# Kernel tuning notes

Measured on AMD Instinct MI355X. Metric: run time of the kernel, lower is better.

The kernel has to match this reference:

```python
import jax, jax.numpy as jnp
import numpy as np

H = 128          # hid_feats
IN0, IN1 = 128, 64
OUT = 64         # out_feats
L = 3            # num_layers
N = 50000        # nodes per graph


def _rbf(x, W, b):
    # sklearn RBFSampler: z = sqrt(2/D) * cos(x @ W + b)
    return jnp.sqrt(2.0 / H) * jnp.cos(x @ W + b)


def _sage_branch(feat, src, dst, Wself, Wneigh, bias, n_nodes):
    # deg of each dst node (constant across layers)
    deg = jax.ops.segment_sum(jnp.ones_like(dst, dtype=feat.dtype), dst, n_nodes)
    denom = jnp.maximum(deg, 1.0)[:, None]
    for i in range(Wself.shape[0]):
        s = jax.ops.segment_sum(feat[src], dst, n_nodes)   # gather + scatter-add
        neigh = jnp.where(deg[:, None] > 0, s / denom, 0.0)
        feat = feat @ Wself[i] + neigh @ Wneigh[i] + bias[i]
    return feat


def setup_inputs() -> dict:
    key = jax.random.key(0)
    ks = jax.random.split(key, 20)
    gamma = 0.1
    inp = {}
    inp['feat0'] = jax.random.normal(ks[0], (N, IN0), jnp.float32)
    inp['feat1'] = jax.random.normal(ks[1], (N, IN1), jnp.float32)
    E = 800000
    inp['src0'] = jax.random.randint(ks[2], (E,), 0, N, jnp.int32)
    inp['dst0'] = jax.random.randint(ks[3], (E,), 0, N, jnp.int32)
    inp['src1'] = jax.random.randint(ks[4], (E,), 0, N, jnp.int32)
    inp['dst1'] = jax.random.randint(ks[5], (E,), 0, N, jnp.int32)
    # RBF random Fourier feature params (W ~ sqrt(2*gamma)*N(0,1), b ~ U[0,2pi))
    inp['rbf_W0'] = jnp.sqrt(2 * gamma) * jax.random.normal(ks[6], (IN0, H), jnp.float32)
    inp['rbf_b0'] = jax.random.uniform(ks[7], (H,), jnp.float32, 0.0, 2 * np.pi)
    inp['rbf_W1'] = jnp.sqrt(2 * gamma) * jax.random.normal(ks[8], (IN1, H), jnp.float32)
    inp['rbf_b1'] = jax.random.uniform(ks[9], (H,), jnp.float32, 0.0, 2 * np.pi)
    sc = 1.0 / np.sqrt(H)
    # branch 1 (g1) and branch 2 (g0) SAGEConv params, stacked over layers
    inp['Wself1'] = sc * jax.random.normal(ks[10], (L, H, H), jnp.float32)
    inp['Wneigh1'] = sc * jax.random.normal(ks[11], (L, H, H), jnp.float32)
    inp['b1'] = jnp.zeros((L, H), jnp.float32)
    inp['Wself2'] = sc * jax.random.normal(ks[12], (L, H, H), jnp.float32)
    inp['Wneigh2'] = sc * jax.random.normal(ks[13], (L, H, H), jnp.float32)
    inp['b2'] = jnp.zeros((L, H), jnp.float32)
    inp['fc1_W'] = sc * jax.random.normal(ks[14], (2 * H, H), jnp.float32)
    inp['fc1_b'] = jnp.zeros((H,), jnp.float32)
    inp['out_W'] = sc * jax.random.normal(ks[15], (H, OUT), jnp.float32)
    inp['out_b'] = jnp.zeros((OUT,), jnp.float32)
    inp['ro_W'] = (1.0 / np.sqrt(OUT)) * jax.random.normal(ks[16], (OUT, 1), jnp.float32)
    inp['ro_b'] = jnp.zeros((1,), jnp.float32)
    return inp


def reference(feat0, feat1, src0, dst0, src1, dst1,
              rbf_W0, rbf_b0, rbf_W1, rbf_b1,
              Wself1, Wneigh1, b1, Wself2, Wneigh2, b2,
              fc1_W, fc1_b, out_W, out_b, ro_W, ro_b):
    # branch 1: g1 path-complex features
    h1 = _rbf(feat1, rbf_W1, rbf_b1)
    y1 = _sage_branch(h1, src1, dst1, Wself1, Wneigh1, b1, feat1.shape[0])
    # branch 2: g0 node features
    h0 = _rbf(feat0, rbf_W0, rbf_b0)
    y2 = _sage_branch(h0, src0, dst0, Wself2, Wneigh2, b2, feat0.shape[0])
    # adaptive_avg_pool1d to 1 == mean over nodes
    y = jnp.concatenate([y2.mean(axis=0), y1.mean(axis=0)], axis=0)  # [2H]
    h = jax.nn.relu(y @ fc1_W + fc1_b)          # dropout is identity in eval
    h = jax.nn.leaky_relu(h @ out_W + out_b, negative_slope=0.01)
    return h @ ro_W + ro_b                      # [1]
```

## Files before the change

kernel.cpp:

```cpp
#include <hip/hip_runtime.h>
#include <math.h>

#define HF   128
#define CAPW 64
#define HB   64

__global__ __launch_bounds__(256) void hist_kernel(const int* __restrict__ s0, const int* __restrict__ d0,
                                                   const int* __restrict__ s1, const int* __restrict__ d1,
                                                   unsigned int* __restrict__ cntbuf,
                                                   int N, int E){
  __shared__ unsigned int sm32[12544];
  const int t = threadIdx.x;
  const int HW = (N + 3) >> 2;
  const int b  = blockIdx.x & 63;
  const int br = (blockIdx.x >> 6) & 1;
  const int z  = blockIdx.x >> 7;
  const int* keys = z ? (br ? d1 : d0) : (br ? s1 : s0);
  for (int w = t; w < HW; w += 256) sm32[w] = 0u;
  __syncthreads();
  const int C  = (E + HB - 1) / HB;
  const int lo = b * C;
  int hi = lo + C; if (hi > E) hi = E;
  for (int i = lo + t; i < hi; i += 256){
    int k = keys[i];
    atomicAdd(&sm32[k >> 2], 1u << ((k & 3) << 3));
  }
  __syncthreads();
  unsigned int* out = cntbuf + ((size_t)(z * 2 + br) * HB + b) * HW;
  for (int w = t; w < HW; w += 256) out[w] = sm32[w];
}

__global__ __launch_bounds__(256) void scan_kernel(unsigned int* __restrict__ cntbuf,
                                                   int* __restrict__ deg,
                                                   int* __restrict__ fill,
                                                   double* __restrict__ SG, int N){
  if (blockIdx.x == 0){
    for (int z = threadIdx.x; z < 1056; z += 256) SG[z] = 0.0;
  }
  int k = blockIdx.x * 256 + threadIdx.x;
  if (k >= 2 * N) return;
  const int br = k >= N;
  const int kk = k - br * N;
  const int HW = (N + 3) >> 2;
  unsigned char* cb = (unsigned char*)cntbuf;
  size_t dbase = ((size_t)(2 + br) * HB) * HW * 4 + kk;
  int ds = 0;
  for (int b = 0; b < HB; ++b) ds += cb[dbase + (size_t)b * HW * 4];
  deg[k] = ds;
  size_t sbase = ((size_t)(0 + br) * HB) * HW * 4 + kk;
  int run = 0;
  for (int b = 0; b < HB; ++b){
    size_t a = sbase + (size_t)b * HW * 4;
    int c = cb[a];
    cb[a] = (unsigned char)run;
    run += c;
  }
  fill[k] = run;
}

__global__ __launch_bounds__(256) void scatter_kernel(const int* __restrict__ s0, const int* __restrict__ d0,
                                                      const int* __restrict__ s1, const int* __restrict__ d1,
                                                      const unsigned int* __restrict__ cntbuf,
                                                      unsigned short* __restrict__ slots,
                                                      int N, int E){
  __shared__ unsigned int sm32[6272];
  const int t  = threadIdx.x;
  const int b  = blockIdx.x & 63;
  const int br = (blockIdx.x >> 6) & 1;
  const int h  = blockIdx.x >> 7;
  const int HW = (N + 3) >> 2;
  const int HN = ((N + 7) >> 3) << 2;
  const int klo = h ? HN : 0;
  const int khi = h ? N : HN;
  const int nw  = (khi - klo + 3) >> 2;
  const unsigned int* offw = cntbuf + ((size_t)br * HB + b) * HW + (klo >> 2);
  for (int w = t; w < nw; w += 256) sm32[w] = offw[w];
  __syncthreads();
  const int* srcA = br ? s1 : s0;
  const int* dstA = br ? d1 : d0;
  const int C  = (E + HB - 1) / HB;
  const int lo = b * C;
  int hi = lo + C; if (hi > E) hi = E;
  const size_t obase = (size_t)br * N;
  for (int i = lo + t; i < hi; i += 256){
    int s = srcA[i];
    if (s < klo || s >= khi) continue;
    int d = dstA[i];
    int sl = s - klo;
    unsigned int old = atomicAdd(&sm32[sl >> 2], 1u << ((sl & 3) << 3));
    int j = (old >> ((sl & 3) << 3)) & 0xff;
    if (j < CAPW) slots[(obase + s) * CAPW + j] = (unsigned short)d;
  }
}

__global__ __launch_bounds__(256) void pull1_kernel(const unsigned short* __restrict__ slots,
                                                    const int* __restrict__ fill,
                                                    const int* __restrict__ deg,
                                                    float* __restrict__ w1,
                                                    float* __restrict__ qa,
                                                    double* __restrict__ S, int N){
  int i = blockIdx.x * 256 + threadIdx.x;
  int t = threadIdx.x;
  float a = 0.f;
  int dgi = 0;
  int br = 0;
  bool valid = i < 2 * N;
  if (valid){
    br = i >= N;
    int o = br * N;
    int c = fill[i]; if (c > CAPW) c = CAPW;
    const unsigned short* sl = slots + (size_t)i * CAPW;
    int j = 0;
    for (; j + 7 < c; j += 8){
      int dA = sl[j], dB = sl[j+1], dC = sl[j+2], dD = sl[j+3];
      int dE = sl[j+4], dF = sl[j+5], dG = sl[j+6], dH = sl[j+7];
      a += 1.f/(float)deg[o+dA] + 1.f/(float)deg[o+dB]
         + 1.f/(float)deg[o+dC] + 1.f/(float)deg[o+dD]
         + 1.f/(float)deg[o+dE] + 1.f/(float)deg[o+dF]
         + 1.f/(float)deg[o+dG] + 1.f/(float)deg[o+dH];
    }
    for (; j < c; ++j) a += 1.f/(float)deg[o + sl[j]];
    dgi = deg[i];
    w1[i] = a;
    qa[i] = dgi > 0 ? a * (1.f/(float)dgi) : 0.f;
  }
  __shared__ double rd[4][256];
  bool pos = valid && dgi > 0;
  rd[0][t] = (pos && !br) ? 1.0 : 0.0;
  rd[1][t] = (pos && !br) ? (double)a : 0.0;
  rd[2][t] = (pos &&  br) ? 1.0 : 0.0;
  rd[3][t] = (pos &&  br) ? (double)a : 0.0;
  __syncthreads();
  for (int off = 128; off; off >>= 1){
    if (t < off){
      rd[0][t] += rd[0][t+off]; rd[1][t] += rd[1][t+off];
      rd[2][t] += rd[2][t+off]; rd[3][t] += rd[3][t+off];
    }
    __syncthreads();
  }
  if (t < 4) atomicAdd(&S[t], rd[t][0]);
}

template<bool WQ>
__global__ __launch_bounds__(256) void pull_kernel(const unsigned short* __restrict__ slots,
                                                   const int* __restrict__ fill,
                                                   const int* __restrict__ deg,
                                                   const float* __restrict__ qin,
                                                   float* __restrict__ wout,
                                                   float* __restrict__ qout, int N){
  int i = blockIdx.x * 256 + threadIdx.x;
  if (i >= 2 * N) return;
  int br = i >= N;
  int o = br * N;
  int c = fill[i]; if (c > CAPW) c = CAPW;
  const unsigned short* sl = slots + (size_t)i * CAPW;
  float a = 0.f;
  int j = 0;
  for (; j + 7 < c; j += 8){
    int dA = sl[j], dB = sl[j+1], dC = sl[j+2], dD = sl[j+3];
    int dE = sl[j+4], dF = sl[j+5], dG = sl[j+6], dH = sl[j+7];
    a += qin[o+dA] + qin[o+dB] + qin[o+dC] + qin[o+dD]
       + qin[o+dE] + qin[o+dF] + qin[o+dG] + qin[o+dH];
  }
  for (; j < c; ++j) a += qin[o + sl[j]];
  wout[i] = a;
  if (WQ){
    int dgi = deg[i];
    qout[i] = dgi > 0 ? a * (1.f/(float)dgi) : 0.f;
  }
}

template<int K1>
__device__ __forceinline__ void gemmred_body(const float* __restrict__ A,
                                             const float* __restrict__ W,
                                             const float* __restrict__ bias,
                                             const float* __restrict__ w1,
                                             const float* __restrict__ w2,
                                             const float* __restrict__ w3,
                                             int wo, float* __restrict__ partial,
                                             int rb, int N,
                                             float (*As)[68], float (*Bs)[132], float (*red)[256]){
  const int t  = threadIdx.x;
  const int tx = t & 15;
  const int ty = t >> 4;
  const int rowbase = rb << 6;

  float acc[4][8];
  #pragma unroll
  for (int i = 0; i < 4; ++i)
    #pragma unroll
    for (int j = 0; j < 8; ++j) acc[i][j] = 0.f;

  const int ar = t >> 2;
  const int ac = (t & 3) << 2;
  const int arow = rowbase + ar;
  const int bk0 = t >> 5;
  const int bc0 = (t & 31) << 2;

  for (int k0 = 0; k0 < K1; k0 += 32){
    __syncthreads();
    float4 av0 = make_float4(0.f,0.f,0.f,0.f), av1 = make_float4(0.f,0.f,0.f,0.f);
    if (arow < N){
      av0 = *(const float4*)&A[(size_t)arow * K1 + (k0 + ac)];
      av1 = *(const float4*)&A[(size_t)arow * K1 + (k0 + 16 + ac)];
    }
    As[ac + 0][ar]      = av0.x; As[ac + 1][ar]      = av0.y;
    As[ac + 2][ar]      = av0.z; As[ac + 3][ar]      = av0.w;
    As[16 + ac + 0][ar] = av1.x; As[16 + ac + 1][ar] = av1.y;
    As[16 + ac + 2][ar] = av1.z; As[16 + ac + 3][ar] = av1.w;
    #pragma unroll
    for (int r = 0; r < 4; ++r)
      *(float4*)&Bs[bk0 + 8*r][bc0] =
        *(const float4*)&W[(size_t)(k0 + bk0 + 8*r) * HF + bc0];
    __syncthreads();
    #pragma unroll
    for (int kk = 0; kk < 32; ++kk){
      const float4 a  = *(const float4*)&As[kk][ty << 2];
      const float4 p0 = *(const float4*)&Bs[kk][tx << 2];
      const float4 p1 = *(const float4*)&Bs[kk][64 + (tx << 2)];
      const float aa[4] = {a.x, a.y, a.z, a.w};
      const float bb[8] = {p0.x, p0.y, p0.z, p0.w, p1.x, p1.y, p1.z, p1.w};
      #pragma unroll
      for (int i = 0; i < 4; ++i)
        #pragma unroll
        for (int j = 0; j < 8; ++j)
          acc[i][j] = fmaf(aa[i], bb[j], acc[i][j]);
    }
  }

  const float4 bia0 = *(const float4*)&bias[tx << 2];
  const float4 bia1 = *(const float4*)&bias[64 + (tx << 2)];
  const float bb0[8] = {bia0.x, bia0.y, bia0.z, bia0.w, bia1.x, bia1.y, bia1.z, bia1.w};
  float o[4][8];
  float wr[4][4];
  #pragma unroll
  for (int i = 0; i < 4; ++i){
    int row = rowbase + (ty << 2) + i;
    bool valid = row < N;
    #pragma unroll
    for (int j = 0; j < 8; ++j)
      o[i][j] = 0.125f * __cosf(acc[i][j] + bb0[j]);
    wr[0][i] = valid ? 1.f : 0.f;
    wr[1][i] = valid ? w1[wo + row] : 0.f;
    wr[2][i] = valid ? w2[wo + row] : 0.f;
    wr[3][i] = valid ? w3[wo + row] : 0.f;
  }
  __syncthreads();
  #pragma unroll
  for (int kp = 0; kp < 2; ++kp){
    const int kA = kp * 2, kB = kp * 2 + 1;
    float cwA[8], cwB[8];
    #pragma unroll
    for (int j = 0; j < 8; ++j){
      cwA[j] = wr[kA][0]*o[0][j] + wr[kA][1]*o[1][j] + wr[kA][2]*o[2][j] + wr[kA][3]*o[3][j];
      cwB[j] = wr[kB][0]*o[0][j] + wr[kB][1]*o[1][j] + wr[kB][2]*o[2][j] + wr[kB][3]*o[3][j];
    }
    #pragma unroll
    for (int j = 0; j < 4; ++j){
      red[ty][(tx << 2) + j]        = cwA[j];
      red[ty][64 + (tx << 2) + j]   = cwA[4 + j];
      red[ty][128 + (tx << 2) + j]  = cwB[j];
      red[ty][192 + (tx << 2) + j]  = cwB[4 + j];
    }
    __syncthreads();
    for (int off = 8; off; off >>= 1){
      if (ty < off){
        #pragma unroll
        for (int j = 0; j < 4; ++j){
          red[ty][(tx << 2) + j]       += red[ty + off][(tx << 2) + j];
          red[ty][64 + (tx << 2) + j]  += red[ty + off][64 + (tx << 2) + j];
          red[ty][128 + (tx << 2) + j] += red[ty + off][128 + (tx << 2) + j];
          red[ty][192 + (tx << 2) + j] += red[ty + off][192 + (tx << 2) + j];
        }
      }
      __syncthreads();
    }
    if (ty == 0){
      #pragma unroll
      for (int j = 0; j < 4; ++j){
        partial[(size_t)rb * 512 + kA * 128 + (tx << 2) + j]      = red[0][(tx << 2) + j];
        partial[(size_t)rb * 512 + kA * 128 + 64 + (tx << 2) + j] = red[0][64 + (tx << 2) + j];
        partial[(size_t)rb * 512 + kB * 128 + (tx << 2) + j]      = red[0][128 + (tx << 2) + j];
        partial[(size_t)rb * 512 + kB * 128 + 64 + (tx << 2) + j] = red[0][192 + (tx << 2) + j];
      }
    }
    __syncthreads();
  }
}

__global__ __launch_bounds__(256) void gemmred2_kernel(const float* __restrict__ A0,
                                                       const float* __restrict__ W0,
                                                       const float* __restrict__ b0,
                                                       const float* __restrict__ A1,
                                                       const float* __restrict__ W1,
                                                       const float* __restrict__ b1,
                                                       const float* __restrict__ w1,
                                                       const float* __restrict__ w2,
                                                       const float* __restrict__ w3,
                                                       float* __restrict__ partial,
                                                       int N, int gg){
  __shared__ __align__(16) float smem[6400];
  float (*As)[68]   = (float(*)[68])smem;
  float (*Bs)[132]  = (float(*)[132])(smem + 2176);
  float (*red)[256] = (float(*)[256])smem;
  if ((int)blockIdx.x < gg)
    gemmred_body<128>(A0, W0, b0, w1, w2, w3, 0, partial, blockIdx.x, N, As, Bs, red);
  else
    gemmred_body<64>(A1, W1, b1, w1, w2, w3, N, partial + (size_t)gg * 512,
                     blockIdx.x - gg, N, As, Bs, red);
}

__global__ __launch_bounds__(512) void greduce_kernel(const float* __restrict__ partial,
                                                      double* __restrict__ G, int nb, int stride){
  int br = blockIdx.y;
  const float* p = partial + (size_t)br * stride;
  double* Gb = G + 512 * br;
  int t = threadIdx.x;
  double s = 0.0;
  for (int b = blockIdx.x; b < nb; b += gridDim.x) s += (double)p[(size_t)b * 512 + t];
  atomicAdd(&Gb[t], s);
}

__global__ __launch_bounds__(512) void head_kernel(const double* __restrict__ G,
                                                   const double* __restrict__ S,
                                                   const float* __restrict__ WsA, const float* __restrict__ WnA, const float* __restrict__ bA,
                                                   const float* __restrict__ WsB, const float* __restrict__ WnB, const float* __restrict__ bB,
                                                   float* __restrict__ ymean, int n){
  const int br = blockIdx.x;
  const double* Gb = G + 512 * br;
  const double* Sb = S + 2 * br;
  const float* Ws   = br ? WsB : WsA;
  const float* Wn   = br ? WnB : WnA;
  const float* bias = br ? bB  : bA;
  float* yout = ymean + 128 * br;

  __shared__ double g[4][128], ng[3][128];
  __shared__ float lws[32][128], lwn[32][128];
  const int t = threadIdx.x;
  const int k = t >> 7, j = t & 127;
  g[k][j] = Gb[t];
  double s[4];
  s[0] = (double)n; s[1] = Sb[0]; s[2] = Sb[1]; s[3] = 0.0;

  for (int i = 0; i < 3; ++i){
    const float* ws = Ws + (size_t)i * 16384;
    const float* wn = Wn + (size_t)i * 16384;
    const float* bi = bias + (size_t)i * 128;
    const int kmax = 2 - i;
    double a = (k <= kmax) ? s[k] * (double)bi[j] : 0.0;
    for (int mc = 0; mc < 128; mc += 32){
      __syncthreads();
      #pragma unroll
      for (int pp = 0; pp < 2; ++pp){
        int idx = (pp * 512 + t) << 2;
        int mm = idx >> 7, cc = idx & 127;
        *(float4*)&lws[mm][cc] = *(const float4*)&ws[(size_t)(mc + mm) * 128 + cc];
        *(float4*)&lwn[mm][cc] = *(const float4*)&wn[(size_t)(mc + mm) * 128 + cc];
      }
      __syncthreads();
      if (k <= kmax){
        #pragma unroll
        for (int m = 0; m < 32; ++m){
          a += g[k][mc + m]     * (double)lws[m][j];
          a += g[k + 1][mc + m] * (double)lwn[m][j];
        }
      }
    }
    __syncthreads();
    if (k <= kmax) ng[k][j] = a;
    __syncthreads();
    if (k <= kmax) g[k][j] = ng[k][j];
  }
  __syncthreads();
  if (t < 128) yout[t] = (float)(g[0][t] / (double)n);
}

__global__ void final_kernel(const float* __restrict__ ymean,
                             const float* __restrict__ fc1W, const float* __restrict__ fc1b,
                             const float* __restrict__ outW, const float* __restrict__ outb,
                             const float* __restrict__ roW, const float* __restrict__ rob,
                             float* __restrict__ out){
  __shared__ float y[256], h1[128], h2[64];
  int t = threadIdx.x;
  y[t] = ymean[t];
  __syncthreads();
  if (t < 128){
    float a = fc1b[t];
    for (int k = 0; k < 256; ++k) a = fmaf(y[k], fc1W[k * 128 + t], a);
    h1[t] = a > 0.f ? a : 0.f;
  }
  __syncthreads();
  if (t < 64){
    float a = outb[t];
    for (int k = 0; k < 128; ++k) a = fmaf(h1[k], outW[k * 64 + t], a);
    h2[t] = a > 0.f ? a : 0.01f * a;
  }
  __syncthreads();
  if (t == 0){
    float a = rob[0];
    for (int k = 0; k < 64; ++k) a = fmaf(h2[k], roW[k], a);
    out[0] = a;
  }
}

extern "C" void kernel_launch(void* const* d_in, const int* in_sizes, int n_in,
                              void* d_out, int out_size, void* d_ws, size_t ws_size,
                              hipStream_t stream){
  const float* feat0  = (const float*)d_in[0];
  const float* feat1  = (const float*)d_in[1];
  const int*   src0   = (const int*)d_in[2];
  const int*   dst0   = (const int*)d_in[3];
  const int*   src1   = (const int*)d_in[4];
  const int*   dst1   = (const int*)d_in[5];
  const float* rbfW0  = (const float*)d_in[6];
  const float* rbfb0  = (const float*)d_in[7];
  const float* rbfW1  = (const float*)d_in[8];
  const float* rbfb1  = (const float*)d_in[9];
  const float* Wself1 = (const float*)d_in[10];
  const float* Wneigh1= (const float*)d_in[11];
  const float* b1     = (const float*)d_in[12];
  const float* Wself2 = (const float*)d_in[13];
  const float* Wneigh2= (const float*)d_in[14];
  const float* b2     = (const float*)d_in[15];
  const float* fc1W   = (const float*)d_in[16];
  const float* fc1b   = (const float*)d_in[17];
  const float* outW   = (const float*)d_in[18];
  const float* outb   = (const float*)d_in[19];
  const float* roW    = (const float*)d_in[20];
  const float* rob    = (const float*)d_in[21];

  const int N = in_sizes[0] / 128;
  const int E = in_sizes[2];
  const int HW = (N + 3) >> 2;

  char* w = (char*)d_ws;
  size_t off = 0;
  auto alloc = [&](size_t bytes) -> char* {
    char* p = w + off; off += (bytes + 255) & ~(size_t)255; return p;
  };
  int*    deg    = (int*)   alloc((size_t)2 * N * 4);
  int*    fill   = (int*)   alloc((size_t)2 * N * 4);
  float*  w1     = (float*) alloc((size_t)2 * N * 4);
  float*  w2     = (float*) alloc((size_t)2 * N * 4);
  float*  w3     = (float*) alloc((size_t)2 * N * 4);
  float*  qa     = (float*) alloc((size_t)2 * N * 4);
  float*  qb     = (float*) alloc((size_t)2 * N * 4);
  double* S      = (double*)alloc(4 * sizeof(double));
  double* G      = (double*)alloc(1024 * sizeof(double));
  float*  ymean  = (float*) alloc(256 * sizeof(float));
  const int gg   = (N + 63) >> 6;
  float*  partial= (float*) alloc((size_t)2 * gg * 512 * 4);
  unsigned short* slots = (unsigned short*)alloc((size_t)2 * N * CAPW * 2);
  unsigned int* cntbuf  = (unsigned int*)alloc((size_t)4 * HB * HW * 4);

  const int nGrid2 = (2 * N + 255) >> 8;

  hist_kernel<<<256, 256, 0, stream>>>(src0, dst0, src1, dst1, cntbuf, N, E);
  scan_kernel<<<nGrid2, 256, 0, stream>>>(cntbuf, deg, fill, S, N);
  scatter_kernel<<<256, 256, 0, stream>>>(src0, dst0, src1, dst1, cntbuf, slots, N, E);
  pull1_kernel<<<nGrid2, 256, 0, stream>>>(slots, fill, deg, w1, qa, S, N);
  pull_kernel<true ><<<nGrid2, 256, 0, stream>>>(slots, fill, deg, qa, w2, qb, N);
  pull_kernel<false><<<nGrid2, 256, 0, stream>>>(slots, fill, deg, qb, w3, qb, N);
  gemmred2_kernel<<<2 * gg, 256, 0, stream>>>(feat0, rbfW0, rbfb0, feat1, rbfW1, rbfb1,
                                              w1, w2, w3, partial, N, gg);
  greduce_kernel<<<dim3(16, 2), 512, 0, stream>>>(partial, G, gg, gg * 512);
  head_kernel<<<2, 512, 0, stream>>>(G, S, Wself2, Wneigh2, b2, Wself1, Wneigh1, b1, ymean, N);
  final_kernel<<<1, 256, 0, stream>>>(ymean, fc1W, fc1b, outW, outb, roW, rob, (float*)d_out);
}
```

Baseline: 197.1 us.

## Fuse graph build and pull passes into one cooperative kernel with grid syncs

Six kernels (histogram, scan, scatter, and three pull passes) become a single cooperative kernel of 256 blocks that separates the phases with grid.sync. This removes five kernel launch gaps. In exchange, the scan and pull phases now run on only 256 blocks in grid-stride loops instead of roughly 390 blocks, so those phases get less parallelism. Grid-wide barriers also add their own synchronisation cost.

New measurement: 380.2 us. +92.9%, slower.

```diff
diff --git a/kernel.cpp b/kernel.cpp
--- a/kernel.cpp
+++ b/kernel.cpp
@@ -1,172 +1,178 @@
 #include <hip/hip_runtime.h>
+#include <hip/hip_cooperative_groups.h>
 #include <math.h>
+
+namespace cg = cooperative_groups;
 
 #define HF   128
 #define CAPW 64
 #define HB   64
 
-__global__ __launch_bounds__(256) void hist_kernel(const int* __restrict__ s0, const int* __restrict__ d0,
+__global__ __launch_bounds__(256) void fused_build(const int* __restrict__ s0, const int* __restrict__ d0,
                                                    const int* __restrict__ s1, const int* __restrict__ d1,
                                                    unsigned int* __restrict__ cntbuf,
+                                                   int* __restrict__ deg, int* __restrict__ fill,
+                                                   double* __restrict__ SG,
+                                                   unsigned short* __restrict__ slots,
+                                                   float* __restrict__ w1, float* __restrict__ qa,
+                                                   float* __restrict__ qb,
+                                                   float* __restrict__ w2, float* __restrict__ w3,
                                                    int N, int E){
-  __shared__ unsigned int sm32[12544];
-  const int t = threadIdx.x;
+  cg::grid_group grid = cg::this_grid();
+  __shared__ __align__(16) unsigned int sm32[12544];
+  const int t  = threadIdx.x;
   const int HW = (N + 3) >> 2;
-  const int b  = blockIdx.x & 63;
-  const int br = (blockIdx.x >> 6) & 1;
-  const int z  = blockIdx.x >> 7;
-  const int* keys = z ? (br ? d1 : d0) : (br ? s1 : s0);
-  for (int w = t; w < HW; w += 256) sm32[w] = 0u;
-  __syncthreads();
   const int C  = (E + HB - 1) / HB;
-  const int lo = b * C;
-  int hi = lo + C; if (hi > E) hi = E;
-  for (int i = lo + t; i < hi; i += 256){
-    int k = keys[i];
-    atomicAdd(&sm32[k >> 2], 1u << ((k & 3) << 3));
-  }
-  __syncthreads();
-  unsigned int* out = cntbuf + ((size_t)(z * 2 + br) * HB + b) * HW;
-  for (int w = t; w < HW; w += 256) out[w] = sm32[w];
-}
-
-__global__ __launch_bounds__(256) void scan_kernel(unsigned int* __restrict__ cntbuf,
-                                                   int* __restrict__ deg,
-                                                   int* __restrict__ fill,
-                                                   double* __restrict__ SG, int N){
-  if (blockIdx.x == 0){
-    for (int z = threadIdx.x; z < 1056; z += 256) SG[z] = 0.0;
-  }
-  int k = blockIdx.x * 256 + threadIdx.x;
-  if (k >= 2 * N) return;
-  const int br = k >= N;
-  const int kk = k - br * N;
-  const int HW = (N + 3) >> 2;
-  unsigned char* cb = (unsigned char*)cntbuf;
-  size_t dbase = ((size_t)(2 + br) * HB) * HW * 4 + kk;
-  int ds = 0;
-  for (int b = 0; b < HB; ++b) ds += cb[dbase + (size_t)b * HW * 4];
-  deg[k] = ds;
-  size_t sbase = ((size_t)(0 + br) * HB) * HW * 4 + kk;
-  int run = 0;
-  for (int b = 0; b < HB; ++b){
-    size_t a = sbase + (size_t)b * HW * 4;
-    int c = cb[a];
-    cb[a] = (unsigned char)run;
-    run += c;
-  }
-  fill[k] = run;
-}
-
-__global__ __launch_bounds__(256) void scatter_kernel(const int* __restrict__ s0, const int* __restrict__ d0,
-                                                      const int* __restrict__ s1, const int* __restrict__ d1,
-                                                      const unsigned int* __restrict__ cntbuf,
-                                                      unsigned short* __restrict__ slots,
-                                                      int N, int E){
-  __shared__ unsigned int sm32[6272];
-  const int t  = threadIdx.x;
-  const int b  = blockIdx.x & 63;
-  const int br = (blockIdx.x >> 6) & 1;
-  const int h  = blockIdx.x >> 7;
-  const int HW = (N + 3) >> 2;
-  const int HN = ((N + 7) >> 3) << 2;
-  const int klo = h ? HN : 0;
-  const int khi = h ? N : HN;
-  const int nw  = (khi - klo + 3) >> 2;
-  const unsigned int* offw = cntbuf + ((size_t)br * HB + b) * HW + (klo >> 2);
-  for (int w = t; w < nw; w += 256) sm32[w] = offw[w];
-  __syncthreads();
-  const int* srcA = br ? s1 : s0;
-  const int* dstA = br ? d1 : d0;
-  const int C  = (E + HB - 1) / HB;
-  const int lo = b * C;
-  int hi = lo + C; if (hi > E) hi = E;
-  const size_t obase = (size_t)br * N;
-  for (int i = lo + t; i < hi; i += 256){
-    int s = srcA[i];
-    if (s < klo || s >= khi) continue;
-    int d = dstA[i];
-    int sl = s - klo;
-    unsigned int old = atomicAdd(&sm32[sl >> 2], 1u << ((sl & 3) << 3));
-    int j = (old >> ((sl & 3) << 3)) & 0xff;
-    if (j < CAPW) slots[(obase + s) * CAPW + j] = (unsigned short)d;
-  }
-}
-
-__global__ __launch_bounds__(256) void pull1_kernel(const unsigned short* __restrict__ slots,
-                                                    const int* __restrict__ fill,
-                                                    const int* __restrict__ deg,
-                                                    float* __restrict__ w1,
-                                                    float* __restrict__ qa,
-                                                    double* __restrict__ S, int N){
-  int i = blockIdx.x * 256 + threadIdx.x;
-  int t = threadIdx.x;
-  float a = 0.f;
-  int dgi = 0;
-  int br = 0;
-  bool valid = i < 2 * N;
-  if (valid){
-    br = i >= N;
+
+  {
+    const int b  = blockIdx.x & 63;
+    const int br = (blockIdx.x >> 6) & 1;
+    const int z  = blockIdx.x >> 7;
+    const int* keys = z ? (br ? d1 : d0) : (br ? s1 : s0);
+    for (int w = t; w < HW; w += 256) sm32[w] = 0u;
+    __syncthreads();
+    const int lo = b * C;
+    int hi = lo + C; if (hi > E) hi = E;
+    for (int i = lo + t; i < hi; i += 256){
+      int k = keys[i];
+      atomicAdd(&sm32[k >> 2], 1u << ((k & 3) << 3));
+    }
+    __syncthreads();
+    unsigned int* out = cntbuf + ((size_t)(z * 2 + br) * HB + b) * HW;
+    for (int w = t; w < HW; w += 256) out[w] = sm32[w];
+  }
+  grid.sync();
+
+  if (blockIdx.x == 0)
+    for (int z = t; z < 1056; z += 256) SG[z] = 0.0;
+  {
+    unsigned char* cb = (unsigned char*)cntbuf;
+    for (int k = blockIdx.x * 256 + t; k < 2 * N; k += gridDim.x * 256){
+      const int br = k >= N;
+      const int kk = k - br * N;
+      size_t dbase = ((size_t)(2 + br) * HB) * HW * 4 + kk;
+      int ds = 0;
+      for (int b = 0; b < HB; ++b) ds += cb[dbase + (size_t)b * HW * 4];
+      deg[k] = ds;
+      size_t sbase = ((size_t)(0 + br) * HB) * HW * 4 + kk;
+      int run = 0;
+      for (int b = 0; b < HB; ++b){
+        size_t a = sbase + (size_t)b * HW * 4;
+        int c = cb[a];
+        cb[a] = (unsigned char)run;
+        run += c;
+      }
+      fill[k] = run;
+    }
+  }
+  grid.sync();
+
+  {
+    const int b  = blockIdx.x & 63;
+    const int br = (blockIdx.x >> 6) & 1;
+    const int h  = blockIdx.x >> 7;
+    const int HN = ((N + 7) >> 3) << 2;
+    const int klo = h ? HN : 0;
+    const int khi = h ? N : HN;
+    const int nw  = (khi - klo + 3) >> 2;
+    const unsigned int* offw = cntbuf + ((size_t)br * HB + b) * HW + (klo >> 2);
+    for (int w = t; w < nw; w += 256) sm32[w] = offw[w];
+    __syncthreads();
+    const int* srcA = br ? s1 : s0;
+    const int* dstA = br ? d1 : d0;
+    const int lo = b * C;
+    int hi = lo + C; if (hi > E) hi = E;
+    const size_t obase = (size_t)br * N;
+    for (int i = lo + t; i < hi; i += 256){
+      int s = srcA[i];
+      if (s < klo || s >= khi) continue;
+      int d = dstA[i];
+      int sl = s - klo;
+      unsigned int old = atomicAdd(&sm32[sl >> 2], 1u << ((sl & 3) << 3));
+      int j = (old >> ((sl & 3) << 3)) & 0xff;
+      if (j < CAPW) slots[(obase + s) * CAPW + j] = (unsigned short)d;
+    }
+  }
+  grid.sync();
+
+  {
+    double r0 = 0.0, r1 = 0.0, r2 = 0.0, r3 = 0.0;
+    for (int i = blockIdx.x * 256 + t; i < 2 * N; i += gridDim.x * 256){
+      int br = i >= N;
+      int o = br * N;
+      int c = fill[i]; if (c > CAPW) c = CAPW;
+      const unsigned short* sl = slots + (size_t)i * CAPW;
+      float a = 0.f;
+      int j = 0;
+      for (; j + 7 < c; j += 8){
+        int dA = sl[j], dB = sl[j+1], dC = sl[j+2], dD = sl[j+3];
+        int dE = sl[j+4], dF = sl[j+5], dG = sl[j+6], dH = sl[j+7];
+        a += 1.f/(float)deg[o+dA] + 1.f/(float)deg[o+dB]
+           + 1.f/(float)deg[o+dC] + 1.f/(float)deg[o+dD]
+           + 1.f/(float)deg[o+dE] + 1.f/(float)deg[o+dF]
+           + 1.f/(float)deg[o+dG] + 1.f/(float)deg[o+dH];
+      }
+      for (; j < c; ++j) a += 1.f/(float)deg[o + sl[j]];
+      int dgi = deg[i];
+      w1[i] = a;
+      qa[i] = dgi > 0 ? a * (1.f/(float)dgi) : 0.f;
+      if (dgi > 0){
+        if (!br){ r0 += 1.0; r1 += (double)a; }
+        else    { r2 += 1.0; r3 += (double)a; }
+      }
+    }
+    double* rd = (double*)sm32;
+    __syncthreads();
+    rd[0*256 + t] = r0; rd[1*256 + t] = r1; rd[2*256 + t] = r2; rd[3*256 + t] = r3;
+    __syncthreads();
+    for (int off = 128; off; off >>= 1){
+      if (t < off){
+        rd[t]       += rd[t + off];
+        rd[256 + t] += rd[256 + t + off];
+        rd[512 + t] += rd[512 + t + off];
+        rd[768 + t] += rd[768 + t + off];
+      }
+      __syncthreads();
+    }
+    if (t < 4) atomicAdd(&SG[t], rd[t * 256]);
+  }
+  grid.sync();
+
+  for (int i = blockIdx.x * 256 + t; i < 2 * N; i += gridDim.x * 256){
+    int br = i >= N;
     int o = br * N;
     int c = fill[i]; if (c > CAPW) c = CAPW;
     const unsigned short* sl = slots + (size_t)i * CAPW;
+    float a = 0.f;
     int j = 0;
     for (; j + 7 < c; j += 8){
       int dA = sl[j], dB = sl[j+1], dC = sl[j+2], dD = sl[j+3];
       int dE = sl[j+4], dF = sl[j+5], dG = sl[j+6], dH = sl[j+7];
-      a += 1.f/(float)deg[o+dA] + 1.f/(float)deg[o+dB]
-         + 1.f/(float)deg[o+dC] + 1.f/(float)deg[o+dD]
-         + 1.f/(float)deg[o+dE] + 1.f/(float)deg[o+dF]
-         + 1.f/(float)deg[o+dG] + 1.f/(float)deg[o+dH];
-    }
-    for (; j < c; ++j) a += 1.f/(float)deg[o + sl[j]];
-    dgi = deg[i];
-    w1[i] = a;
-    qa[i] = dgi > 0 ? a * (1.f/(float)dgi) : 0.f;
-  }
-  __shared__ double rd[4][256];
-  bool pos = valid && dgi > 0;
-  rd[0][t] = (pos && !br) ? 1.0 : 0.0;
-  rd[1][t] = (pos && !br) ? (double)a : 0.0;
-  rd[2][t] = (pos &&  br) ? 1.0 : 0.0;
-  rd[3][t] = (pos &&  br) ? (double)a : 0.0;
-  __syncthreads();
-  for (int off = 128; off; off >>= 1){
-    if (t < off){
-      rd[0][t] += rd[0][t+off]; rd[1][t] += rd[1][t+off];
-      rd[2][t] += rd[2][t+off]; rd[3][t] += rd[3][t+off];
-    }
-    __syncthreads();
-  }
-  if (t < 4) atomicAdd(&S[t], rd[t][0]);
-}
-
-template<bool WQ>
-__global__ __launch_bounds__(256) void pull_kernel(const unsigned short* __restrict__ slots,
-                                                   const int* __restrict__ fill,
-                                                   const int* __restrict__ deg,
-                                                   const float* __restrict__ qin,
-                                                   float* __restrict__ wout,
-                                                   float* __restrict__ qout, int N){
-  int i = blockIdx.x * 256 + threadIdx.x;
-  if (i >= 2 * N) return;
-  int br = i >= N;
-  int o = br * N;
-  int c = fill[i]; if (c > CAPW) c = CAPW;
-  const unsigned short* sl = slots + (size_t)i * CAPW;
-  float a = 0.f;
-  int j = 0;
-  for (; j + 7 < c; j += 8){
-    int dA = sl[j], dB = sl[j+1], dC = sl[j+2], dD = sl[j+3];
-    int dE = sl[j+4], dF = sl[j+5], dG = sl[j+6], dH = sl[j+7];
-    a += qin[o+dA] + qin[o+dB] + qin[o+dC] + qin[o+dD]
-       + qin[o+dE] + qin[o+dF] + qin[o+dG] + qin[o+dH];
-  }
-  for (; j < c; ++j) a += qin[o + sl[j]];
-  wout[i] = a;
-  if (WQ){
+      a += qa[o+dA] + qa[o+dB] + qa[o+dC] + qa[o+dD]
+         + qa[o+dE] + qa[o+dF] + qa[o+dG] + qa[o+dH];
+    }
+    for (; j < c; ++j) a += qa[o + sl[j]];
+    w2[i] = a;
     int dgi = deg[i];
-    qout[i] = dgi > 0 ? a * (1.f/(float)dgi) : 0.f;
+    qb[i] = dgi > 0 ? a * (1.f/(float)dgi) : 0.f;
+  }
+  grid.sync();
+
+  for (int i = blockIdx.x * 256 + t; i < 2 * N; i += gridDim.x * 256){
+    int br = i >= N;
+    int o = br * N;
+    int c = fill[i]; if (c > CAPW) c = CAPW;
+    const unsigned short* sl = slots + (size_t)i * CAPW;
+    float a = 0.f;
+    int j = 0;
+    for (; j + 7 < c; j += 8){
+      int dA = sl[j], dB = sl[j+1], dC = sl[j+2], dD = sl[j+3];
+      int dE = sl[j+4], dF = sl[j+5], dG = sl[j+6], dH = sl[j+7];
+      a += qb[o+dA] + qb[o+dB] + qb[o+dC] + qb[o+dD]
+         + qb[o+dE] + qb[o+dF] + qb[o+dG] + qb[o+dH];
+    }
+    for (; j < c; ++j) a += qb[o + sl[j]];
+    w3[i] = a;
   }
 }
 
@@ -453,14 +459,15 @@
   unsigned short* slots = (unsigned short*)alloc((size_t)2 * N * CAPW * 2);
   unsigned int* cntbuf  = (unsigned int*)alloc((size_t)4 * HB * HW * 4);
 
-  const int nGrid2 = (2 * N + 255) >> 8;
-
-  hist_kernel<<<256, 256, 0, stream>>>(src0, dst0, src1, dst1, cntbuf, N, E);
-  scan_kernel<<<nGrid2, 256, 0, stream>>>(cntbuf, deg, fill, S, N);
-  scatter_kernel<<<256, 256, 0, stream>>>(src0, dst0, src1, dst1, cntbuf, slots, N, E);
-  pull1_kernel<<<nGrid2, 256, 0, stream>>>(slots, fill, deg, w1, qa, S, N);
-  pull_kernel<true ><<<nGrid2, 256, 0, stream>>>(slots, fill, deg, qa, w2, qb, N);
-  pull_kernel<false><<<nGrid2, 256, 0, stream>>>(slots, fill, deg, qb, w3, qb, N);
+  {
+    void* args[] = {
+      (void*)&src0, (void*)&dst0, (void*)&src1, (void*)&dst1,
+      (void*)&cntbuf, (void*)&deg, (void*)&fill, (void*)&S,
+      (void*)&slots, (void*)&w1, (void*)&qa, (void*)&qb,
+      (void*)&w2, (void*)&w3, (void*)&N, (void*)&E
+    };
+    hipLaunchCooperativeKernel((void*)fused_build, dim3(256), dim3(256), args, 0, stream);
+  }
   gemmred2_kernel<<<2 * gg, 256, 0, stream>>>(feat0, rbfW0, rbfb0, feat1, rbfW1, rbfb1,
                                               w1, w2, w3, partial, N, gg);
   greduce_kernel<<<dim3(16, 2), 512, 0, stream>>>(partial, G, gg, gg * 512);
```
